# Optimization experiments

Measured on AMD Instinct MI355X. Metric: run time of the kernel, lower is better.

## Reference

```python
import jax, jax.numpy as jnp
import numpy as np

BN_EPSILON = 1e-05


def hard_sigmoid(x):
    return jnp.clip((x + 1.0) / 2.0, 0.0, 1.0)


def setup_inputs() -> dict:
    key = jax.random.key(0)
    kx, kw, kb = jax.random.split(key, 3)
    # NHWC activations
    x = jax.random.normal(kx, (64, 112, 112, 64), dtype=jnp.float32)
    # HWIO kernel initialized ~ truncated_normal(stddev=0.2), then Bernoulli-binarized
    # to +/-1 once at graph-construction time (set_input_shape), so we sample here.
    k_init = 0.2 * jax.random.normal(kw, (3, 3, 64, 64), dtype=jnp.float32)
    kernels = 2.0 * jax.random.bernoulli(kb, hard_sigmoid(k_init)).astype(jnp.float32) - 1.0
    # tf.contrib.layers.batch_norm defaults: center=True (beta), scale=False (no gamma)
    beta = jnp.zeros((64,), dtype=jnp.float32)
    return {"x": x, "kernels": kernels, "beta": beta}


def reference(x, kernels, beta):
    # Training-mode batch norm: per-batch moments over (N, H, W)
    mean = jnp.mean(x, axis=(0, 1, 2))
    var = jnp.var(x, axis=(0, 1, 2))
    x_bn = (x - mean) * jax.lax.rsqrt(var + BN_EPSILON) + beta
    # NOTE: original code computes conv(sign(x_bn), k) but immediately overwrites it
    # with conv(x_bn, k); the effective forward uses the batch-normed (non-signed)
    # activations with the binarized (+/-1) kernels.
    a = jax.lax.conv_general_dilated(
        x_bn, kernels,
        window_strides=(1, 1),
        padding="SAME",
        dimension_numbers=("NHWC", "HWIO", "NHWC"),
    )
    return a
```

## Files before the change

kernel.cpp:

```cpp
#include <hip/hip_runtime.h>

typedef __attribute__((ext_vector_type(8))) short bf16x8;
typedef __attribute__((ext_vector_type(4))) float f32x4;

#define HW      112
#define CH      64
#define PIX_IMG (HW*HW)
#define N4TOT   (64*112*112*64/4)
#define NPIX_F  802816.0f

__device__ __forceinline__ unsigned short f2bf(float f) {
  unsigned u = __float_as_uint(f);
  u += 0x7FFFu + ((u >> 16) & 1u);
  return (unsigned short)(u >> 16);
}

__global__ void zero_ws(float* __restrict__ ws) {
  ws[threadIdx.x] = 0.0f;
}

__global__ __launch_bounds__(256) void stats_kernel(const float* __restrict__ x,
                                                    float* __restrict__ ws) {
  __shared__ float red[128];
  const int tid = threadIdx.x;
  if (tid < 128) red[tid] = 0.0f;
  __syncthreads();

  const float4* __restrict__ x4 = (const float4*)x;
  float4 s = make_float4(0.f, 0.f, 0.f, 0.f);
  float4 q = make_float4(0.f, 0.f, 0.f, 0.f);
  const int stride = gridDim.x * 256;
  #pragma unroll 4
  for (int i = blockIdx.x * 256 + tid; i < N4TOT; i += stride) {
    float4 v = x4[i];
    s.x += v.x; s.y += v.y; s.z += v.z; s.w += v.w;
    q.x = fmaf(v.x, v.x, q.x); q.y = fmaf(v.y, v.y, q.y);
    q.z = fmaf(v.z, v.z, q.z); q.w = fmaf(v.w, v.w, q.w);
  }
  const int c0 = (tid & 15) * 4;
  atomicAdd(&red[c0 + 0], s.x); atomicAdd(&red[c0 + 1], s.y);
  atomicAdd(&red[c0 + 2], s.z); atomicAdd(&red[c0 + 3], s.w);
  atomicAdd(&red[64 + c0 + 0], q.x); atomicAdd(&red[64 + c0 + 1], q.y);
  atomicAdd(&red[64 + c0 + 2], q.z); atomicAdd(&red[64 + c0 + 3], q.w);
  __syncthreads();
  if (tid < 128) atomicAdd(&ws[tid], red[tid]);
}

__global__ void finalize_kernel(const float* __restrict__ beta, float* __restrict__ ws) {
  const int c = threadIdx.x;
  float mean = ws[c] / NPIX_F;
  float var  = ws[64 + c] / NPIX_F - mean * mean;
  var = fmaxf(var, 0.0f);
  float sc = rsqrtf(var + 1e-5f);
  ws[128 + c] = sc;
  ws[192 + c] = beta[c] - mean * sc;
}

__global__ __launch_bounds__(256) void prep_w(const float* __restrict__ k,
                                              unsigned short* __restrict__ wsw) {
  const int idx = blockIdx.x * 256 + threadIdx.x;
  const int tap = idx >> 12;
  const int co  = (idx >> 6) & 63;
  const int ci  = idx & 63;
  wsw[idx] = f2bf(k[(tap * 64 + ci) * 64 + co]);
}

__global__ __launch_bounds__(448, 4) void conv_kernel(const float* __restrict__ x,
                                                      const unsigned short* __restrict__ wsw,
                                                      const float* __restrict__ ws,
                                                      float* __restrict__ out) {
  __shared__ unsigned short Xs[4 * 114 * 72];
  __shared__ unsigned short Wl[64 * 72];
  const int tid = threadIdx.x;
  const int bid = blockIdx.x;
  const int n  = bid / 56;
  const int h0 = (bid % 56) * 2;

  const int f4  = tid & 15;
  const int ci0 = f4 * 4;
  const float4 s4 = *(const float4*)(ws + 128 + ci0);
  const float4 b4 = *(const float4*)(ws + 192 + ci0);

  const int pp0 = tid >> 4;
  for (int ir = 0; ir < 4; ++ir) {
    const int g = h0 - 1 + ir;
    const bool rowok = ((unsigned)g < 112u);
    const float* xrow = x + ((n * 112 + (rowok ? g : 0)) * 112) * 64;
    for (int pp = pp0; pp < 114; pp += 28) {
      const int w = pp - 1;
      float4 v = make_float4(0.f, 0.f, 0.f, 0.f);
      if (rowok && (unsigned)w < 112u) v = *(const float4*)(xrow + w * 64 + ci0);
      ushort4 o;
      o.x = f2bf(fmaf(v.x, s4.x, b4.x));
      o.y = f2bf(fmaf(v.y, s4.y, b4.y));
      o.z = f2bf(fmaf(v.z, s4.z, b4.z));
      o.w = f2bf(fmaf(v.w, s4.w, b4.w));
      *(ushort4*)(&Xs[(ir * 114 + pp) * 72 + ci0]) = o;
    }
  }
  __syncthreads();

  f32x4 acc[2][4];
  #pragma unroll
  for (int r = 0; r < 2; ++r)
    #pragma unroll
    for (int mt = 0; mt < 4; ++mt) acc[r][mt] = (f32x4){0.f, 0.f, 0.f, 0.f};

  const int lane = tid & 63;
  const int wv   = tid >> 6;
  const int qd   = lane >> 4;
  const int cc   = lane & 15;

  for (int tap = 0; tap < 9; ++tap) {
    for (int t = tid; t < 512; t += 448) {
      uint4 val = ((const uint4*)wsw)[tap * 512 + t];
      *((uint4*)(Wl + (t >> 3) * 72 + (t & 7) * 8)) = val;
    }
    __syncthreads();
    const int dh = tap / 3, dw = tap % 3;
    #pragma unroll
    for (int s = 0; s < 2; ++s) {
      const bf16x8 xb0 = *(const bf16x8*)(&Xs[((0 + dh) * 114 + wv * 16 + dw + cc) * 72 + s * 32 + qd * 8]);
      const bf16x8 xb1 = *(const bf16x8*)(&Xs[((1 + dh) * 114 + wv * 16 + dw + cc) * 72 + s * 32 + qd * 8]);
      #pragma unroll
      for (int mt = 0; mt < 4; ++mt) {
        const bf16x8 wa = *(const bf16x8*)(&Wl[(mt * 16 + cc) * 72 + s * 32 + qd * 8]);
        acc[0][mt] = __builtin_amdgcn_mfma_f32_16x16x32_bf16(wa, xb0, acc[0][mt], 0, 0, 0);
        acc[1][mt] = __builtin_amdgcn_mfma_f32_16x16x32_bf16(wa, xb1, acc[1][mt], 0, 0, 0);
      }
    }
    __syncthreads();
  }

  #pragma unroll
  for (int r = 0; r < 2; ++r) {
    const int pix = n * PIX_IMG + (h0 + r) * 112 + wv * 16 + cc;
    float* op = out + pix * 64 + qd * 4;
    #pragma unroll
    for (int mt = 0; mt < 4; ++mt) {
      *(f32x4*)(op + mt * 16) = acc[r][mt];
    }
  }
}

extern "C" void kernel_launch(void* const* d_in, const int* in_sizes, int n_in,
                              void* d_out, int out_size, void* d_ws, size_t ws_size,
                              hipStream_t stream) {
  const float* x    = (const float*)d_in[0];
  const float* kern = (const float*)d_in[1];
  const float* beta = (const float*)d_in[2];
  float* out = (float*)d_out;
  float* ws  = (float*)d_ws;
  unsigned short* wsw = (unsigned short*)((char*)d_ws + 4096);

  zero_ws<<<1, 128, 0, stream>>>(ws);
  stats_kernel<<<1024, 256, 0, stream>>>(x, ws);
  finalize_kernel<<<1, 64, 0, stream>>>(beta, ws);
  prep_w<<<144, 256, 0, stream>>>(kern, wsw);
  conv_kernel<<<64 * 56, 448, 0, stream>>>(x, wsw, ws, out);
}
```

Baseline: 509.7 us.

## Fold batch-norm into conv weights and bias, stage bf16 input copy

Batch-norm scale is folded into the bf16 weights and the shift into a per-output bias computed from the kernel sums. Padding is filled with a value that maps to zero after normalization, so the conv reads raw activations. When the workspace is large enough, the stats pass also writes a bf16 copy of x so the conv reads half the bytes. The conv tile grows to four output rows per block with double-buffered weights per kernel row, and the stats reduction uses wave shuffles before the LDS atomics. The cost is an extra write of the bf16 copy and rounding the padding value and the per-channel scale into bf16 weights.

Result: faster. 483.8 us (-5.1%).

```diff
diff --git a/kernel.cpp b/kernel.cpp
--- a/kernel.cpp
+++ b/kernel.cpp
@@ -1,6 +1,7 @@
 #include <hip/hip_runtime.h>
 
 typedef __attribute__((ext_vector_type(8))) short bf16x8;
+typedef __attribute__((ext_vector_type(8))) unsigned short u16x8;
 typedef __attribute__((ext_vector_type(4))) float f32x4;
 
 #define HW      112
@@ -9,6 +10,10 @@
 #define N4TOT   (64*112*112*64/4)
 #define NPIX_F  802816.0f
 
+#define WS_HV_BYTE  1280
+#define WS_W_BYTE   4096
+#define WS_XBF_BYTE (4u<<20)
+
 __device__ __forceinline__ unsigned short f2bf(float f) {
   unsigned u = __float_as_uint(f);
   u += 0x7FFFu + ((u >> 16) & 1u);
@@ -19,8 +24,10 @@
   ws[threadIdx.x] = 0.0f;
 }
 
+template <bool WRITE_BF>
 __global__ __launch_bounds__(256) void stats_kernel(const float* __restrict__ x,
-                                                    float* __restrict__ ws) {
+                                                    float* __restrict__ ws,
+                                                    unsigned short* __restrict__ xbf) {
   __shared__ float red[128];
   const int tid = threadIdx.x;
   if (tid < 128) red[tid] = 0.0f;
@@ -36,110 +43,172 @@
     s.x += v.x; s.y += v.y; s.z += v.z; s.w += v.w;
     q.x = fmaf(v.x, v.x, q.x); q.y = fmaf(v.y, v.y, q.y);
     q.z = fmaf(v.z, v.z, q.z); q.w = fmaf(v.w, v.w, q.w);
-  }
-  const int c0 = (tid & 15) * 4;
-  atomicAdd(&red[c0 + 0], s.x); atomicAdd(&red[c0 + 1], s.y);
-  atomicAdd(&red[c0 + 2], s.z); atomicAdd(&red[c0 + 3], s.w);
-  atomicAdd(&red[64 + c0 + 0], q.x); atomicAdd(&red[64 + c0 + 1], q.y);
-  atomicAdd(&red[64 + c0 + 2], q.z); atomicAdd(&red[64 + c0 + 3], q.w);
+    if (WRITE_BF) {
+      ushort4 o;
+      o.x = f2bf(v.x); o.y = f2bf(v.y); o.z = f2bf(v.z); o.w = f2bf(v.w);
+      *(ushort4*)(xbf + 4 * i) = o;
+    }
+  }
+  #pragma unroll
+  for (int m = 16; m <= 32; m <<= 1) {
+    s.x += __shfl_xor(s.x, m); s.y += __shfl_xor(s.y, m);
+    s.z += __shfl_xor(s.z, m); s.w += __shfl_xor(s.w, m);
+    q.x += __shfl_xor(q.x, m); q.y += __shfl_xor(q.y, m);
+    q.z += __shfl_xor(q.z, m); q.w += __shfl_xor(q.w, m);
+  }
+  if ((tid & 63) < 16) {
+    const int c0 = (tid & 15) * 4;
+    atomicAdd(&red[c0 + 0], s.x); atomicAdd(&red[c0 + 1], s.y);
+    atomicAdd(&red[c0 + 2], s.z); atomicAdd(&red[c0 + 3], s.w);
+    atomicAdd(&red[64 + c0 + 0], q.x); atomicAdd(&red[64 + c0 + 1], q.y);
+    atomicAdd(&red[64 + c0 + 2], q.z); atomicAdd(&red[64 + c0 + 3], q.w);
+  }
   __syncthreads();
   if (tid < 128) atomicAdd(&ws[tid], red[tid]);
 }
 
-__global__ void finalize_kernel(const float* __restrict__ beta, float* __restrict__ ws) {
-  const int c = threadIdx.x;
-  float mean = ws[c] / NPIX_F;
-  float var  = ws[64 + c] / NPIX_F - mean * mean;
-  var = fmaxf(var, 0.0f);
-  float sc = rsqrtf(var + 1e-5f);
-  ws[128 + c] = sc;
-  ws[192 + c] = beta[c] - mean * sc;
+__global__ __launch_bounds__(256) void finalize_kernel(const float* __restrict__ beta,
+                                                       const float* __restrict__ k,
+                                                       float* __restrict__ ws) {
+  __shared__ float sb[64];
+  __shared__ float part[256];
+  const int tid = threadIdx.x;
+  if (tid < 64) {
+    float mean = ws[tid] * (1.0f / NPIX_F);
+    float var  = fmaxf(ws[64 + tid] * (1.0f / NPIX_F) - mean * mean, 0.0f);
+    float sc = rsqrtf(var + 1e-5f);
+    float b  = beta[tid] - mean * sc;
+    ws[128 + tid] = sc;
+    ws[192 + tid] = b;
+    ((unsigned short*)((char*)ws + WS_HV_BYTE))[tid] = f2bf(-b / sc);
+    sb[tid] = b;
+  }
+  __syncthreads();
+  const int co = tid & 63, pt = tid >> 6;
+  float a = 0.f;
+  #pragma unroll 8
+  for (int t = pt; t < 576; t += 4)
+    a = fmaf(sb[t & 63], k[t * 64 + co], a);
+  part[tid] = a;
+  __syncthreads();
+  if (tid < 64)
+    ws[256 + tid] = part[tid] + part[64 + tid] + part[128 + tid] + part[192 + tid];
 }
 
 __global__ __launch_bounds__(256) void prep_w(const float* __restrict__ k,
+                                              const float* __restrict__ ws,
                                               unsigned short* __restrict__ wsw) {
-  const int idx = blockIdx.x * 256 + threadIdx.x;
-  const int tap = idx >> 12;
-  const int co  = (idx >> 6) & 63;
-  const int ci  = idx & 63;
-  wsw[idx] = f2bf(k[(tap * 64 + ci) * 64 + co]);
-}
-
+  const int oidx = blockIdx.x * 256 + threadIdx.x;
+  const int j  = oidx & 7;
+  const int co = (oidx >> 3) & 63;
+  const int qd = (oidx >> 9) & 3;
+  const int t2 = oidx >> 11;
+  const int tap = t2 % 9;
+  const int h   = t2 / 9;
+  const int ci  = h * 32 + qd * 8 + j;
+  wsw[oidx] = f2bf(k[(tap * 64 + ci) * 64 + co] * ws[128 + ci]);
+}
+
+template <bool USE_BF>
 __global__ __launch_bounds__(448, 4) void conv_kernel(const float* __restrict__ x,
+                                                      const unsigned short* __restrict__ xbf,
                                                       const unsigned short* __restrict__ wsw,
                                                       const float* __restrict__ ws,
                                                       float* __restrict__ out) {
-  __shared__ unsigned short Xs[4 * 114 * 72];
-  __shared__ unsigned short Wl[64 * 72];
+  __shared__ unsigned short Xs[6 * 114 * 40];
+  __shared__ unsigned short Wd[2 * 6144];
   const int tid = threadIdx.x;
   const int bid = blockIdx.x;
-  const int n  = bid / 56;
-  const int h0 = (bid % 56) * 2;
-
-  const int f4  = tid & 15;
-  const int ci0 = f4 * 4;
-  const float4 s4 = *(const float4*)(ws + 128 + ci0);
-  const float4 b4 = *(const float4*)(ws + 192 + ci0);
-
-  const int pp0 = tid >> 4;
-  for (int ir = 0; ir < 4; ++ir) {
-    const int g = h0 - 1 + ir;
-    const bool rowok = ((unsigned)g < 112u);
-    const float* xrow = x + ((n * 112 + (rowok ? g : 0)) * 112) * 64;
-    for (int pp = pp0; pp < 114; pp += 28) {
-      const int w = pp - 1;
-      float4 v = make_float4(0.f, 0.f, 0.f, 0.f);
-      if (rowok && (unsigned)w < 112u) v = *(const float4*)(xrow + w * 64 + ci0);
-      ushort4 o;
-      o.x = f2bf(fmaf(v.x, s4.x, b4.x));
-      o.y = f2bf(fmaf(v.y, s4.y, b4.y));
-      o.z = f2bf(fmaf(v.z, s4.z, b4.z));
-      o.w = f2bf(fmaf(v.w, s4.w, b4.w));
-      *(ushort4*)(&Xs[(ir * 114 + pp) * 72 + ci0]) = o;
-    }
-  }
-  __syncthreads();
-
-  f32x4 acc[2][4];
-  #pragma unroll
-  for (int r = 0; r < 2; ++r)
-    #pragma unroll
-    for (int mt = 0; mt < 4; ++mt) acc[r][mt] = (f32x4){0.f, 0.f, 0.f, 0.f};
+  const int n  = bid / 28;
+  const int h0 = (bid % 28) * 4;
 
   const int lane = tid & 63;
   const int wv   = tid >> 6;
   const int qd   = lane >> 4;
   const int cc   = lane & 15;
-
-  for (int tap = 0; tap < 9; ++tap) {
-    for (int t = tid; t < 512; t += 448) {
-      uint4 val = ((const uint4*)wsw)[tap * 512 + t];
-      *((uint4*)(Wl + (t >> 3) * 72 + (t & 7) * 8)) = val;
-    }
+  const int wvb  = wv * 16;
+
+  const unsigned short* hv = (const unsigned short*)((const char*)ws + WS_HV_BYTE);
+
+  f32x4 acc[4][4];
+  {
+    const float* bo = ws + 256;
+    #pragma unroll
+    for (int mt = 0; mt < 4; ++mt) {
+      const f32x4 bv = *(const f32x4*)(bo + mt * 16 + qd * 4);
+      #pragma unroll
+      for (int r = 0; r < 4; ++r) acc[r][mt] = bv;
+    }
+  }
+
+  for (int half = 0; half < 2; ++half) {
+    {
+      u16x8 hv8[4];
+      #pragma unroll
+      for (int o = 0; o < 4; ++o) hv8[o] = *(const u16x8*)(hv + half * 32 + o * 8);
+      for (int c = tid; c < 2736; c += 448) {
+        const int o  = c & 3;
+        const int pi = c >> 2;
+        const int p  = pi % 114;
+        const int r  = pi / 114;
+        const int w  = p - 1;
+        const int g  = h0 + r - 1;
+        u16x8 v;
+        if ((unsigned)w < 112u && (unsigned)g < 112u) {
+          const int base = ((n * 112 + g) * 112 + w) * 64 + half * 32 + o * 8;
+          if (USE_BF) {
+            v = *(const u16x8*)(xbf + base);
+          } else {
+            const float* sp = x + base;
+            const float4 a = *(const float4*)sp;
+            const float4 b = *(const float4*)(sp + 4);
+            v = (u16x8){f2bf(a.x), f2bf(a.y), f2bf(a.z), f2bf(a.w),
+                        f2bf(b.x), f2bf(b.y), f2bf(b.z), f2bf(b.w)};
+          }
+        } else {
+          v = hv8[o];
+        }
+        *(u16x8*)(&Xs[pi * 40 + o * 8]) = v;
+      }
+    }
+    const unsigned short* wh = wsw + half * 18432;
+    for (int t = tid; t < 768; t += 448)
+      *(u16x8*)(&Wd[t * 8]) = *(const u16x8*)(wh + t * 8);
     __syncthreads();
-    const int dh = tap / 3, dw = tap % 3;
-    #pragma unroll
-    for (int s = 0; s < 2; ++s) {
-      const bf16x8 xb0 = *(const bf16x8*)(&Xs[((0 + dh) * 114 + wv * 16 + dw + cc) * 72 + s * 32 + qd * 8]);
-      const bf16x8 xb1 = *(const bf16x8*)(&Xs[((1 + dh) * 114 + wv * 16 + dw + cc) * 72 + s * 32 + qd * 8]);
+
+    for (int dh = 0; dh < 3; ++dh) {
+      if (dh < 2) {
+        const unsigned short* ws_src = wh + (dh + 1) * 6144;
+        const int nb = ((dh + 1) & 1) * 6144;
+        for (int t = tid; t < 768; t += 448)
+          *(u16x8*)(&Wd[nb + t * 8]) = *(const u16x8*)(ws_src + t * 8);
+      }
+      const int cb = (dh & 1) * 6144;
       #pragma unroll
-      for (int mt = 0; mt < 4; ++mt) {
-        const bf16x8 wa = *(const bf16x8*)(&Wl[(mt * 16 + cc) * 72 + s * 32 + qd * 8]);
-        acc[0][mt] = __builtin_amdgcn_mfma_f32_16x16x32_bf16(wa, xb0, acc[0][mt], 0, 0, 0);
-        acc[1][mt] = __builtin_amdgcn_mfma_f32_16x16x32_bf16(wa, xb1, acc[1][mt], 0, 0, 0);
+      for (int dw = 0; dw < 3; ++dw) {
+        bf16x8 xb[4];
+        #pragma unroll
+        for (int r = 0; r < 4; ++r)
+          xb[r] = *(const bf16x8*)(&Xs[((r + dh) * 114 + wvb + dw + cc) * 40 + qd * 8]);
+        #pragma unroll
+        for (int mt = 0; mt < 4; ++mt) {
+          const bf16x8 wa = *(const bf16x8*)(&Wd[cb + ((dw * 4 + qd) * 64 + mt * 16 + cc) * 8]);
+          #pragma unroll
+          for (int r = 0; r < 4; ++r)
+            acc[r][mt] = __builtin_amdgcn_mfma_f32_16x16x32_bf16(wa, xb[r], acc[r][mt], 0, 0, 0);
+        }
       }
-    }
-    __syncthreads();
+      __syncthreads();
+    }
   }
 
   #pragma unroll
-  for (int r = 0; r < 2; ++r) {
-    const int pix = n * PIX_IMG + (h0 + r) * 112 + wv * 16 + cc;
+  for (int r = 0; r < 4; ++r) {
+    const int pix = n * PIX_IMG + (h0 + r) * 112 + wvb + cc;
     float* op = out + pix * 64 + qd * 4;
     #pragma unroll
-    for (int mt = 0; mt < 4; ++mt) {
+    for (int mt = 0; mt < 4; ++mt)
       *(f32x4*)(op + mt * 16) = acc[r][mt];
-    }
   }
 }
 
@@ -151,11 +220,16 @@
   const float* beta = (const float*)d_in[2];
   float* out = (float*)d_out;
   float* ws  = (float*)d_ws;
-  unsigned short* wsw = (unsigned short*)((char*)d_ws + 4096);
+  unsigned short* wsw = (unsigned short*)((char*)d_ws + WS_W_BYTE);
+  unsigned short* xbf = (unsigned short*)((char*)d_ws + WS_XBF_BYTE);
+
+  const bool use_bf = ws_size >= (size_t)WS_XBF_BYTE + 102760448ull;
 
   zero_ws<<<1, 128, 0, stream>>>(ws);
-  stats_kernel<<<1024, 256, 0, stream>>>(x, ws);
-  finalize_kernel<<<1, 64, 0, stream>>>(beta, ws);
-  prep_w<<<144, 256, 0, stream>>>(kern, wsw);
-  conv_kernel<<<64 * 56, 448, 0, stream>>>(x, wsw, ws, out);
-}
+  if (use_bf) stats_kernel<true ><<<1024, 256, 0, stream>>>(x, ws, xbf);
+  else        stats_kernel<false><<<1024, 256, 0, stream>>>(x, ws, xbf);
+  finalize_kernel<<<1, 256, 0, stream>>>(beta, kern, ws);
+  prep_w<<<144, 256, 0, stream>>>(kern, ws, wsw);
+  if (use_bf) conv_kernel<true ><<<64 * 28, 448, 0, stream>>>(x, xbf, wsw, ws, out);
+  else        conv_kernel<false><<<64 * 28, 448, 0, stream>>>(x, xbf, wsw, ws, out);
+}
```
